# Performance work log

Measured on AMD Instinct MI355X. Metric: run time of the kernel, lower is better.

## Reference

```python
import jax, jax.numpy as jnp
import numpy as np

MARGIN = 0.5
AP_VALUE = 0.8
AN_VALUE = 0.4
ABS_W = 1.0


def setup_inputs() -> dict:
    key = jax.random.key(0)
    k1, k2 = jax.random.split(key)
    bs, d = 16384, 64
    inputs = jax.random.normal(k1, (bs, d), dtype=jnp.float32)
    target = jax.random.randint(k2, (bs,), 0, 64, dtype=jnp.int64)
    return {"inputs": inputs, "target": target}


def reference(inputs, target):
    # L2-normalize features (normalize_feature=True)
    x = inputs / jnp.linalg.norm(inputs, axis=-1, keepdims=True)

    # cross-entropy on normalized features treated as logits
    logp = jax.nn.log_softmax(x, axis=-1)  # [bs, d]
    loss_ce = -jnp.mean(jnp.take_along_axis(logp, target[:, None], axis=1))

    # cosine-similarity matrix [bs, bs]
    dist = x @ x.T

    is_pos = target[None, :] == target[:, None]
    # hard mining: min similarity among positives, max among negatives (per row)
    dist_ap = jnp.min(jnp.where(is_pos, dist, jnp.inf), axis=1)   # [bs]
    dist_an = jnp.max(jnp.where(is_pos, -jnp.inf, dist), axis=1)  # [bs]

    loss = jnp.mean(jax.nn.relu(MARGIN + dist_ap - dist_an))

    # absolute (angular margin) terms
    abs_ap = jax.nn.relu(AP_VALUE - dist_ap)
    abs_an = jax.nn.relu(dist_an - AN_VALUE)
    loss = (jnp.mean(abs_an) + jnp.mean(abs_ap)) * ABS_W + loss

    return loss + loss_ce
```

## Files before the change

kernel.cpp:

```cpp
#include <hip/hip_runtime.h>


#define N_ROWS 16384
#define N_DIM 64

typedef __attribute__((ext_vector_type(8))) short bf16x8;
typedef __attribute__((ext_vector_type(4))) float f32x4;

__device__ inline unsigned short f2bf(float f) {
  unsigned u = __float_as_uint(f);
  unsigned r = u + 0x7fffu + ((u >> 16) & 1u);
  return (unsigned short)(r >> 16);
}

__device__ inline unsigned enc_key(float f) {
  unsigned u = __float_as_uint(f);
  return (u & 0x80000000u) ? ~u : (u | 0x80000000u);
}
__device__ inline float dec_key(unsigned k) {
  unsigned u = (k & 0x80000000u) ? (k ^ 0x80000000u) : ~k;
  return __uint_as_float(u);
}

__device__ inline void g2lds16(const void* g, void* l) {
  __builtin_amdgcn_global_load_lds(
      (const __attribute__((address_space(1))) void*)g,
      (__attribute__((address_space(3))) void*)l, 16, 0, 0);
}

__global__ void prep_kernel(const float* __restrict__ x, const int* __restrict__ tgt,
                            unsigned short* __restrict__ xb, float* __restrict__ ce_row) {
  const int row  = blockIdx.x * 4 + (threadIdx.x >> 6);
  const int lane = threadIdx.x & 63;
  float v  = x[row * N_DIM + lane];
  float ss = v * v;
#pragma unroll
  for (int s = 1; s < 64; s <<= 1) ss += __shfl_xor(ss, s, 64);
  float xn = v * rsqrtf(ss);
  xb[row * N_DIM + lane] = f2bf(xn);

  float mx = xn;
#pragma unroll
  for (int s = 1; s < 64; s <<= 1) mx = fmaxf(mx, __shfl_xor(mx, s, 64));
  float e  = __expf(xn - mx);
  float se = e;
#pragma unroll
  for (int s = 1; s < 64; s <<= 1) se += __shfl_xor(se, s, 64);
  float lse = mx + __logf(se);
  int   t   = tgt[row];
  float xt  = __shfl(xn, t, 64);
  if (lane == 0) ce_row[row] = lse - xt;
}

__global__ __launch_bounds__(256, 4)
void mine_kernel(const unsigned short* __restrict__ xb, const int* __restrict__ tgt,
                 unsigned* __restrict__ mp_key, unsigned* __restrict__ mn_key) {
  __shared__ unsigned short Bt[2][1024];
  __shared__ int tjl[N_ROWS / 16];

  const int lane    = threadIdx.x & 63;
  const int wv      = threadIdx.x >> 6;
  const int iblk    = blockIdx.x >> 4;
  const int jspl    = blockIdx.x & 15;
  const int rowbase = iblk * 256 + wv * 64;
  const int m = lane & 15, q = lane >> 4;
  const int jbase = jspl * (N_ROWS / 16);

  bf16x8 a[4][2];
#pragma unroll
  for (int tr = 0; tr < 4; ++tr) {
    const unsigned short* p = xb + (rowbase + tr * 16 + m) * N_DIM + q * 8;
    a[tr][0] = *(const bf16x8*)(p);
    a[tr][1] = *(const bf16x8*)(p + 32);
  }
  int ti[4][4];
#pragma unroll
  for (int tr = 0; tr < 4; ++tr)
#pragma unroll
    for (int r = 0; r < 4; ++r)
      ti[tr][r] = tgt[rowbase + tr * 16 + q * 4 + r];

  float mp[16], mn[16];
#pragma unroll
  for (int k = 0; k < 16; ++k) { mp[k] = __builtin_inff(); mn[k] = -__builtin_inff(); }

  for (int k = threadIdx.x; k < N_ROWS / 16; k += 256) tjl[k] = tgt[jbase + k];

  const unsigned short* srcbase =
      xb + (jbase + wv * 8 + (lane >> 3)) * N_DIM +
      (((lane & 7) ^ ((lane >> 3) & 7)) * 8);

  if (wv < 2) g2lds16(srcbase, &Bt[0][wv * 512]);
  __syncthreads();

  const int roff0 = m * 128 + ((q * 16) ^ ((m & 7) << 4));
  const int roff1 = m * 128 + (((64) + q * 16) ^ ((m & 7) << 4));

  for (int jc = 0; jc < 64; ++jc) {
    const int p = jc & 1;
    if (wv < 2 && jc < 63)
      g2lds16(srcbase + (jc + 1) * 16 * N_DIM, &Bt[p ^ 1][wv * 512]);

    const char* bb = (const char*)&Bt[p][0];
    const bf16x8 cb0 = *(const bf16x8*)(bb + roff0);
    const bf16x8 cb1 = *(const bf16x8*)(bb + roff1);
    const int    ctj = tjl[jc * 16 + m];

#pragma unroll
    for (int tr = 0; tr < 4; ++tr) {
      f32x4 acc = {0.f, 0.f, 0.f, 0.f};
      acc = __builtin_amdgcn_mfma_f32_16x16x32_bf16(a[tr][0], cb0, acc, 0, 0, 0);
      acc = __builtin_amdgcn_mfma_f32_16x16x32_bf16(a[tr][1], cb1, acc, 0, 0, 0);
#pragma unroll
      for (int r = 0; r < 4; ++r) {
        const bool  pos = (ctj == ti[tr][r]);
        const float d   = acc[r];
        const int   k   = tr * 4 + r;
        mp[k] = fminf(mp[k], pos ? d : __builtin_inff());
        mn[k] = fmaxf(mn[k], pos ? -__builtin_inff() : d);
      }
    }
    __syncthreads();
  }

#pragma unroll
  for (int s = 1; s < 16; s <<= 1) {
#pragma unroll
    for (int k = 0; k < 16; ++k) {
      mp[k] = fminf(mp[k], __shfl_xor(mp[k], s, 64));
      mn[k] = fmaxf(mn[k], __shfl_xor(mn[k], s, 64));
    }
  }
  if (m == 0) {
#pragma unroll
    for (int tr = 0; tr < 4; ++tr)
#pragma unroll
      for (int r = 0; r < 4; ++r) {
        const int row = rowbase + tr * 16 + q * 4 + r;
        atomicMin(&mp_key[row], enc_key(mp[tr * 4 + r]));
        atomicMax(&mn_key[row], enc_key(mn[tr * 4 + r]));
      }
  }
}

__global__ void finalize_kernel(const unsigned* __restrict__ mp_key, const unsigned* __restrict__ mn_key,
                                const float* __restrict__ ce_row, float* __restrict__ out) {
  __shared__ float red[4][16];
  float s1 = 0.f, s2 = 0.f, s3 = 0.f, s4 = 0.f;
  for (int r = threadIdx.x; r < N_ROWS; r += 1024) {
    float ap = dec_key(mp_key[r]);
    float an = dec_key(mn_key[r]);
    s1 += fmaxf(0.5f + ap - an, 0.f);
    s2 += fmaxf(0.8f - ap, 0.f);
    s3 += fmaxf(an - 0.4f, 0.f);
    s4 += ce_row[r];
  }
#pragma unroll
  for (int s = 1; s < 64; s <<= 1) {
    s1 += __shfl_xor(s1, s, 64);
    s2 += __shfl_xor(s2, s, 64);
    s3 += __shfl_xor(s3, s, 64);
    s4 += __shfl_xor(s4, s, 64);
  }
  const int wv = threadIdx.x >> 6;
  if ((threadIdx.x & 63) == 0) {
    red[0][wv] = s1; red[1][wv] = s2; red[2][wv] = s3; red[3][wv] = s4;
  }
  __syncthreads();
  if (threadIdx.x == 0) {
    float t = 0.f;
#pragma unroll
    for (int c = 0; c < 4; ++c) {
      float tc = 0.f;
#pragma unroll
      for (int w = 0; w < 16; ++w) tc += red[c][w];
      t += tc;
    }
    out[0] = t * (1.0f / N_ROWS);
  }
}

extern "C" void kernel_launch(void* const* d_in, const int* in_sizes, int n_in,
                              void* d_out, int out_size, void* d_ws, size_t ws_size,
                              hipStream_t stream) {
  const float* x   = (const float*)d_in[0];
  const int*   tgt = (const int*)d_in[1];
  char* ws = (char*)d_ws;

  unsigned short* xb     = (unsigned short*)ws;
  unsigned*       mp_key = (unsigned*)(ws + (2u << 20));
  unsigned*       mn_key = (unsigned*)(ws + (2u << 20) + (64u << 10));
  float*          ce_row = (float*)(ws + (2u << 20) + (128u << 10));
  float*          out    = (float*)d_out;

  hipMemsetAsync(mp_key, 0xFF, 64u << 10, stream);
  hipMemsetAsync(mn_key, 0x00, 64u << 10, stream);

  prep_kernel<<<N_ROWS / 4, 256, 0, stream>>>(x, tgt, xb, ce_row);
  mine_kernel<<<(N_ROWS / 256) * 16, 256, 0, stream>>>(xb, tgt, mp_key, mn_key);
  finalize_kernel<<<1, 1024, 0, stream>>>(mp_key, mn_key, ce_row, out);
}
```

Baseline: 165.1 us.

## Fold memsets into prep kernel, pack targets, parallelize finalize with atomics

Removes the two hipMemsetAsync calls by having prep_kernel initialize the min/max key buffers and zero the output. Packs four row target labels into one 32-bit register as bytes, which cuts register use in the mining loop at the cost of extra shift/mask ops and relies on labels being below 256. The finalize step now runs on 8 blocks that combine partial sums through an atomicAdd into the output instead of a single block.

```diff
diff --git a/kernel.cpp b/kernel.cpp
--- a/kernel.cpp
+++ b/kernel.cpp
@@ -29,7 +29,9 @@
 }
 
 __global__ void prep_kernel(const float* __restrict__ x, const int* __restrict__ tgt,
-                            unsigned short* __restrict__ xb, float* __restrict__ ce_row) {
+                            unsigned short* __restrict__ xb, float* __restrict__ ce_row,
+                            unsigned* __restrict__ mp_key, unsigned* __restrict__ mn_key,
+                            float* __restrict__ out) {
   const int row  = blockIdx.x * 4 + (threadIdx.x >> 6);
   const int lane = threadIdx.x & 63;
   float v  = x[row * N_DIM + lane];
@@ -49,7 +51,12 @@
   float lse = mx + __logf(se);
   int   t   = tgt[row];
   float xt  = __shfl(xn, t, 64);
-  if (lane == 0) ce_row[row] = lse - xt;
+  if (lane == 0) {
+    ce_row[row] = lse - xt;
+    mp_key[row] = 0xFFFFFFFFu;
+    mn_key[row] = 0u;
+  }
+  if (blockIdx.x == 0 && threadIdx.x == 0) out[0] = 0.f;
 }
 
 __global__ __launch_bounds__(256, 4)
@@ -73,12 +80,15 @@
     a[tr][0] = *(const bf16x8*)(p);
     a[tr][1] = *(const bf16x8*)(p + 32);
   }
-  int ti[4][4];
+  unsigned tip[4];
 #pragma unroll
-  for (int tr = 0; tr < 4; ++tr)
+  for (int tr = 0; tr < 4; ++tr) {
+    unsigned vv = 0;
 #pragma unroll
     for (int r = 0; r < 4; ++r)
-      ti[tr][r] = tgt[rowbase + tr * 16 + q * 4 + r];
+      vv |= ((unsigned)tgt[rowbase + tr * 16 + q * 4 + r] & 0xffu) << (8 * r);
+    tip[tr] = vv;
+  }
 
   float mp[16], mn[16];
 #pragma unroll
@@ -104,7 +114,7 @@
     const char* bb = (const char*)&Bt[p][0];
     const bf16x8 cb0 = *(const bf16x8*)(bb + roff0);
     const bf16x8 cb1 = *(const bf16x8*)(bb + roff1);
-    const int    ctj = tjl[jc * 16 + m];
+    const unsigned ctj = (unsigned)tjl[jc * 16 + m] & 0xffu;
 
 #pragma unroll
     for (int tr = 0; tr < 4; ++tr) {
@@ -113,7 +123,7 @@
       acc = __builtin_amdgcn_mfma_f32_16x16x32_bf16(a[tr][1], cb1, acc, 0, 0, 0);
 #pragma unroll
       for (int r = 0; r < 4; ++r) {
-        const bool  pos = (ctj == ti[tr][r]);
+        const bool  pos = (((tip[tr] >> (8 * r)) & 0xffu) == ctj);
         const float d   = acc[r];
         const int   k   = tr * 4 + r;
         mp[k] = fminf(mp[k], pos ? d : __builtin_inff());
@@ -145,38 +155,26 @@
 
 __global__ void finalize_kernel(const unsigned* __restrict__ mp_key, const unsigned* __restrict__ mn_key,
                                 const float* __restrict__ ce_row, float* __restrict__ out) {
-  __shared__ float red[4][16];
-  float s1 = 0.f, s2 = 0.f, s3 = 0.f, s4 = 0.f;
-  for (int r = threadIdx.x; r < N_ROWS; r += 1024) {
+  __shared__ float red[16];
+  float s = 0.f;
+#pragma unroll
+  for (int it = 0; it < 2; ++it) {
+    const int r = it * 8192 + blockIdx.x * 1024 + threadIdx.x;
     float ap = dec_key(mp_key[r]);
     float an = dec_key(mn_key[r]);
-    s1 += fmaxf(0.5f + ap - an, 0.f);
-    s2 += fmaxf(0.8f - ap, 0.f);
-    s3 += fmaxf(an - 0.4f, 0.f);
-    s4 += ce_row[r];
+    s += fmaxf(0.5f + ap - an, 0.f) + fmaxf(0.8f - ap, 0.f) +
+         fmaxf(an - 0.4f, 0.f) + ce_row[r];
   }
 #pragma unroll
-  for (int s = 1; s < 64; s <<= 1) {
-    s1 += __shfl_xor(s1, s, 64);
-    s2 += __shfl_xor(s2, s, 64);
-    s3 += __shfl_xor(s3, s, 64);
-    s4 += __shfl_xor(s4, s, 64);
-  }
+  for (int sh = 1; sh < 64; sh <<= 1) s += __shfl_xor(s, sh, 64);
   const int wv = threadIdx.x >> 6;
-  if ((threadIdx.x & 63) == 0) {
-    red[0][wv] = s1; red[1][wv] = s2; red[2][wv] = s3; red[3][wv] = s4;
-  }
+  if ((threadIdx.x & 63) == 0) red[wv] = s;
   __syncthreads();
   if (threadIdx.x == 0) {
     float t = 0.f;
 #pragma unroll
-    for (int c = 0; c < 4; ++c) {
-      float tc = 0.f;
-#pragma unroll
-      for (int w = 0; w < 16; ++w) tc += red[c][w];
-      t += tc;
-    }
-    out[0] = t * (1.0f / N_ROWS);
+    for (int w = 0; w < 16; ++w) t += red[w];
+    atomicAdd(out, t * (1.0f / N_ROWS));
   }
 }
 
@@ -193,10 +191,7 @@
   float*          ce_row = (float*)(ws + (2u << 20) + (128u << 10));
   float*          out    = (float*)d_out;
 
-  hipMemsetAsync(mp_key, 0xFF, 64u << 10, stream);
-  hipMemsetAsync(mn_key, 0x00, 64u << 10, stream);
-
-  prep_kernel<<<N_ROWS / 4, 256, 0, stream>>>(x, tgt, xb, ce_row);
+  prep_kernel<<<N_ROWS / 4, 256, 0, stream>>>(x, tgt, xb, ce_row, mp_key, mn_key, out);
   mine_kernel<<<(N_ROWS / 256) * 16, 256, 0, stream>>>(xb, tgt, mp_key, mn_key);
-  finalize_kernel<<<1, 1024, 0, stream>>>(mp_key, mn_key, ce_row, out);
+  finalize_kernel<<<8, 1024, 0, stream>>>(mp_key, mn_key, ce_row, out);
 }
```

Result: no change. 165.4 us (+0.2%).
